# Performance work log

Hardware: AMD Instinct MI355X
Metric: run time of the kernel (lower is better)

## Reference

```python
import jax, jax.numpy as jnp
import numpy as np

N_H = 16
N_KV = 4
D_K = 128
ROPE_BASE = 10000.0


def _rope(t, cos, sin):
    # t: [B, T, H, d_k]; cos/sin: [1, T, 1, d_k//2]
    te, to = t[..., 0::2], t[..., 1::2]
    oe = te * cos - to * sin
    oo = te * sin + to * cos
    return jnp.stack([oe, oo], axis=-1).reshape(t.shape)


def setup_inputs() -> dict:
    key = jax.random.key(0)
    ks = jax.random.split(key, 5)
    B, T, d = 4, 2048, 2048
    s = 0.02
    return {
        "x": jax.random.normal(ks[0], (B, T, d), jnp.float32),
        "Wq": jax.random.normal(ks[1], (d, d), jnp.float32) * s,
        "Wk": jax.random.normal(ks[2], (d, N_KV * D_K), jnp.float32) * s,
        "Wv": jax.random.normal(ks[3], (d, N_KV * D_K), jnp.float32) * s,
        "Wp": jax.random.normal(ks[4], (d, d), jnp.float32) * s,
        "bp": jnp.zeros((d,), jnp.float32),
    }


def reference(x, Wq, Wk, Wv, Wp, bp):
    B, T, C = x.shape
    g = N_H // N_KV  # group size

    q = (x @ Wq).reshape(B, T, N_H, D_K)
    k = (x @ Wk).reshape(B, T, N_KV, D_K)
    v = (x @ Wv).reshape(B, T, N_KV, D_K)

    # RoPE frequencies (constants)
    theta = ROPE_BASE ** (-2.0 * jnp.arange(0, D_K, 2, dtype=jnp.float32) / D_K)
    freq = jnp.arange(T, dtype=jnp.float32)[:, None] * theta[None, :]  # [T, d_k//2]
    cos = jnp.cos(freq)[None, :, None, :]
    sin = jnp.sin(freq)[None, :, None, :]
    q = _rope(q, cos, sin)
    k = _rope(k, cos, sin)

    # GQA: group q heads by shared kv head (equiv to repeat_interleave on kv)
    q = q.reshape(B, T, N_KV, g, D_K).transpose(0, 2, 3, 1, 4)  # [B,n_kv,g,T,d_k]
    k = k.transpose(0, 2, 1, 3)  # [B,n_kv,T,d_k]
    v = v.transpose(0, 2, 1, 3)

    scores = jnp.einsum('bngqd,bnkd->bngqk', q, k) * (D_K ** -0.5)
    causal = jnp.tril(jnp.ones((T, T), bool))
    scores = jnp.where(causal, scores, -jnp.inf)
    attn = jax.nn.softmax(scores, axis=-1)
    out = jnp.einsum('bngqk,bnkd->bngqd', attn, v)  # [B,n_kv,g,T,d_k]
    out = out.transpose(0, 3, 1, 2, 4).reshape(B, T, C)
    return out @ Wp + bp
```

## Files before the change

### kernel.cpp

```cpp
#include <hip/hip_runtime.h>
#include <hip/hip_bf16.h>
#include <math.h>

typedef __bf16 bf16_t;
typedef __bf16 bf16x8 __attribute__((ext_vector_type(8)));
typedef __bf16 bf16x4 __attribute__((ext_vector_type(4)));
typedef float f32x4 __attribute__((ext_vector_type(4)));
typedef float f32x16 __attribute__((ext_vector_type(16)));
typedef unsigned int u32;

#define MFMA16 __builtin_amdgcn_mfma_f32_16x16x32_bf16
#define MFMA32 __builtin_amdgcn_mfma_f32_32x32x16_bf16

static __device__ __forceinline__ u32 pkbf(float a, float b) {
  union { bf16_t h[2]; u32 u; } z;
  z.h[0] = (bf16_t)a; z.h[1] = (bf16_t)b;
  return z.u;
}

static __device__ __forceinline__ void gload16(const bf16_t* g, bf16_t* l) {
  __builtin_amdgcn_global_load_lds(
      (const __attribute__((address_space(1))) void*)g,
      (__attribute__((address_space(3))) void*)l, 16, 0, 0);
}

__global__ void k_f32_to_bf16(const float* __restrict__ in, bf16_t* __restrict__ out, long n) {
  long i = ((long)blockIdx.x * blockDim.x + threadIdx.x) * 4;
  long stride = (long)gridDim.x * blockDim.x * 4;
  for (; i < n; i += stride) {
    const float4 v = *(const float4*)(in + i);
    bf16x4 o; o[0] = (bf16_t)v.x; o[1] = (bf16_t)v.y; o[2] = (bf16_t)v.z; o[3] = (bf16_t)v.w;
    *(bf16x4*)(out + i) = o;
  }
}

__global__ void k_transpose_bf16(const float* __restrict__ W, bf16_t* __restrict__ WT,
                                 int K, int N) {
  __shared__ float tile[32][33];
  int n0 = blockIdx.x * 32, k0 = blockIdx.y * 32;
  int tx = threadIdx.x & 31, ty = threadIdx.x >> 5;
#pragma unroll
  for (int i = 0; i < 4; i++)
    tile[ty + i * 8][tx] = W[(size_t)(k0 + ty + i * 8) * N + n0 + tx];
  __syncthreads();
#pragma unroll
  for (int i = 0; i < 4; i++) {
    int n = ty + i * 8;
    WT[(size_t)(n0 + n) * K + k0 + tx] = (bf16_t)tile[tx][n];
  }
}

__global__ void k_rope(bf16_t* __restrict__ qkv) {
  int idx = blockIdx.x * blockDim.x + threadIdx.x;
  if (idx >= 8192 * 1280) return;
  int r = idx / 1280, p = idx - r * 1280;
  int t = r & 2047;
  int i = p & 63;
  float theta = exp2f(-(float)i * 0.41524101186092029f);
  float f = (float)t * theta;
  float s, c;
  sincosf(f, &s, &c);
  bf16_t* a = qkv + (size_t)r * 3072 + p * 2;
  float e = (float)a[0], o = (float)a[1];
  a[0] = (bf16_t)(e * c - o * s);
  a[1] = (bf16_t)(e * s + o * c);
}

template <bool F32OUT>
__global__ __launch_bounds__(256, 2) void k_gemm_bt(
    const bf16_t* __restrict__ A, const bf16_t* __restrict__ BT,
    bf16_t* __restrict__ Cb, float* __restrict__ Cf,
    const float* __restrict__ bias, int M, int N, int K, int nwg) {
  __shared__ bf16_t sA[128 * 64];
  __shared__ bf16_t sB[128 * 64];
  int nbn = N >> 7;
  int orig = (int)blockIdx.x;
  int swz = (orig & 7) * (nwg >> 3) + (orig >> 3);
  int bm = swz / nbn, bn = swz % nbn;
  int tid = threadIdx.x;
  int lane = tid & 63, wid = tid >> 6;
  int wm = (wid >> 1) << 6, wn = (wid & 1) << 6;
  int lr = lane & 15, lq = lane >> 4;
  f32x4 acc[4][4] = {};

  int srow = wid * 32 + (lane >> 3);
  int scol = (lane & 7) * 8;
  const bf16_t* Ag = A + (size_t)(bm * 128 + srow) * K + scol;
  const bf16_t* Bg = BT + (size_t)(bn * 128 + srow) * K + scol;
  bf16_t* Al = &sA[(wid * 32) * 64];
  bf16_t* Bl = &sB[(wid * 32) * 64];

  for (int k0 = 0; k0 < K; k0 += 64) {
#pragma unroll
    for (int i = 0; i < 4; i++) {
      gload16(Ag + (size_t)i * 8 * K + k0, Al + i * 8 * 64);
      gload16(Bg + (size_t)i * 8 * K + k0, Bl + i * 8 * 64);
    }
    __syncthreads();
#pragma unroll
    for (int kc = 0; kc < 2; kc++) {
      bf16x8 af[4], bfr[4];
#pragma unroll
      for (int m = 0; m < 4; m++)
        af[m] = *(const bf16x8*)&sA[(wm + m * 16 + lr) * 64 + kc * 32 + lq * 8];
#pragma unroll
      for (int n = 0; n < 4; n++)
        bfr[n] = *(const bf16x8*)&sB[(wn + n * 16 + lr) * 64 + kc * 32 + lq * 8];
#pragma unroll
      for (int m = 0; m < 4; m++)
#pragma unroll
        for (int n = 0; n < 4; n++)
          acc[m][n] = MFMA16(af[m], bfr[n], acc[m][n], 0, 0, 0);
    }
    __syncthreads();
  }
#pragma unroll
  for (int m = 0; m < 4; m++) {
    int row0 = bm * 128 + wm + m * 16 + lq * 4;
#pragma unroll
    for (int n = 0; n < 4; n++) {
      int col = bn * 128 + wn + n * 16 + lr;
#pragma unroll
      for (int r = 0; r < 4; r++) {
        if constexpr (F32OUT)
          Cf[(size_t)(row0 + r) * N + col] = acc[m][n][r] + bias[col];
        else
          Cb[(size_t)(row0 + r) * N + col] = (bf16_t)acc[m][n][r];
      }
    }
  }
}

__global__ __launch_bounds__(256, 2) void k_attn(const bf16_t* __restrict__ qkv,
                                                 bf16_t* __restrict__ out) {
  __shared__ bf16_t sK[64 * 128];
  __shared__ bf16_t sVT[128 * 72];
  int bid = blockIdx.x;
  int g = bid >> 6;
  int qt = (g & 1) ? (g >> 1) : (15 - (g >> 1));
  int bh = bid & 63;
  int h = bh & 15, b = bh >> 4;
  int kvh = h >> 2;
  const size_t RS = 3072;
  const bf16_t* Qb = qkv + (size_t)b * 2048 * RS + h * 128;
  const bf16_t* Kb = qkv + (size_t)b * 2048 * RS + 2048 + kvh * 128;
  const bf16_t* Vb = Kb + 512;
  int q0 = qt * 128;
  int tid = threadIdx.x, lane = tid & 63, wid = tid >> 6;
  int l31 = lane & 31, hi = lane >> 5;
  int qw = q0 + wid * 32;

  bf16x8 qf[8];
  {
    const bf16_t* qrow = Qb + (size_t)(qw + l31) * RS + hi * 8;
#pragma unroll
    for (int dc = 0; dc < 8; dc++)
      qf[dc] = *(const bf16x8*)(qrow + dc * 16);
  }

  f32x16 oT[4] = {};
  float m_r = -INFINITY, l_r = 0.f;
  const float SC = 0.08838834764831845f * 1.4426950408889634f;

  int vc = tid & 127, vro = (tid >> 7) * 8;

  int ntiles = 2 * qt + 2;
  for (int kt = 0; kt < ntiles; kt++) {
    int k0 = kt * 64;
#pragma unroll
    for (int ps = 0; ps < 4; ps++) {
      int idx = tid + ps * 256;
      int row = idx >> 4, seg = idx & 15;
      bf16x8 kv = *(const bf16x8*)(Kb + (size_t)(k0 + row) * RS + seg * 8);
      int off = row * 256 + ((seg * 16) ^ ((row & 7) << 4));
      *(bf16x8*)((char*)sK + off) = kv;
    }
#pragma unroll
    for (int i = 0; i < 4; i++) {
      int kr = vro + i * 16;
      bf16x8 vv;
#pragma unroll
      for (int j = 0; j < 8; j++) vv[j] = Vb[(size_t)(k0 + kr + j) * RS + vc];
      *(bf16x8*)&sVT[vc * 72 + kr] = vv;
    }
    __syncthreads();

    if (k0 <= qw + 31) {
      f32x16 sa0 = {}, sa1 = {};
#pragma unroll
      for (int dc = 0; dc < 8; dc++) {
        int cb = (dc * 32 + hi * 16) ^ ((l31 & 7) << 4);
        bf16x8 kf0 = *(const bf16x8*)((const char*)sK + l31 * 256 + cb);
        bf16x8 kf1 = *(const bf16x8*)((const char*)sK + (32 + l31) * 256 + cb);
        sa0 = MFMA32(kf0, qf[dc], sa0, 0, 0, 0);
        sa1 = MFMA32(kf1, qf[dc], sa1, 0, 0, 0);
      }
      float p[2][16];
      int qg = qw + l31;
      float pm = -INFINITY;
#pragma unroll
      for (int nf = 0; nf < 2; nf++)
#pragma unroll
        for (int r = 0; r < 16; r++) {
          int kg = k0 + nf * 32 + (r & 3) + 8 * (r >> 2) + 4 * hi;
          float v = (kg <= qg) ? (nf ? sa1[r] : sa0[r]) * SC : -INFINITY;
          p[nf][r] = v;
          pm = fmaxf(pm, v);
        }
      pm = fmaxf(pm, __shfl_xor(pm, 32));
      bool skip = __all(pm <= m_r + 8.f);
      float mn = skip ? m_r : fmaxf(m_r, pm);
      float alpha = skip ? 1.f : exp2f(m_r - mn);
      m_r = mn;
      float rs = 0.f;
#pragma unroll
      for (int nf = 0; nf < 2; nf++)
#pragma unroll
        for (int r = 0; r < 16; r++) {
          float e = exp2f(p[nf][r] - m_r);
          p[nf][r] = e;
          rs += e;
        }
      rs += __shfl_xor(rs, 32);
      l_r = l_r * alpha + rs;
      if (!skip) {
#pragma unroll
        for (int c = 0; c < 4; c++)
#pragma unroll
          for (int r = 0; r < 16; r++) oT[c][r] *= alpha;
      }
#pragma unroll
      for (int nf = 0; nf < 2; nf++) {
        u32 Qk[4][2];
#pragma unroll
        for (int gg = 0; gg < 4; gg++) {
          Qk[gg][0] = pkbf(p[nf][4 * gg + 0], p[nf][4 * gg + 1]);
          Qk[gg][1] = pkbf(p[nf][4 * gg + 2], p[nf][4 * gg + 3]);
        }
#pragma unroll
        for (int kc = 0; kc < 2; kc++) {
          u32 x0 = __shfl_xor(Qk[2 * kc + 1 - hi][0], 32);
          u32 x1 = __shfl_xor(Qk[2 * kc + 1 - hi][1], 32);
          u32 o0 = Qk[2 * kc + hi][0], o1 = Qk[2 * kc + hi][1];
          union { u32 w[4]; bf16x8 v; } pf;
          pf.w[0] = hi ? x0 : o0;
          pf.w[1] = hi ? x1 : o1;
          pf.w[2] = hi ? o0 : x0;
          pf.w[3] = hi ? o1 : x1;
          int slot = nf * 2 + kc;
#pragma unroll
          for (int c = 0; c < 4; c++) {
            bf16x8 vf = *(const bf16x8*)&sVT[(c * 32 + l31) * 72 + slot * 16 + hi * 8];
            oT[c] = MFMA32(vf, pf.v, oT[c], 0, 0, 0);
          }
        }
      }
    }
    __syncthreads();
  }
  float inv = 1.f / l_r;
  size_t row = (size_t)b * 2048 + qw + l31;
#pragma unroll
  for (int c = 0; c < 4; c++)
#pragma unroll
    for (int rr = 0; rr < 4; rr++) {
      bf16x4 o4;
#pragma unroll
      for (int j = 0; j < 4; j++) o4[j] = (bf16_t)(oT[c][rr * 4 + j] * inv);
      *(bf16x4*)(out + row * 2048 + h * 128 + c * 32 + rr * 8 + hi * 4) = o4;
    }
}

extern "C" void kernel_launch(void* const* d_in, const int* in_sizes, int n_in,
                              void* d_out, int out_size, void* d_ws, size_t ws_size,
                              hipStream_t stream) {
  const float* x = (const float*)d_in[0];
  const float* Wq = (const float*)d_in[1];
  const float* Wk = (const float*)d_in[2];
  const float* Wv = (const float*)d_in[3];
  const float* Wp = (const float*)d_in[4];
  const float* bp = (const float*)d_in[5];
  float* out = (float*)d_out;

  bf16_t* ws = (bf16_t*)d_ws;
  bf16_t* xb = ws;
  bf16_t* qkv = ws + 16777216;
  bf16_t* WqkvT = ws + 16777216 + 25165824;
  bf16_t* WpT = WqkvT + 6291456;

  k_f32_to_bf16<<<2048, 256, 0, stream>>>(x, xb, 16777216L);
  k_transpose_bf16<<<dim3(64, 64), 256, 0, stream>>>(Wq, WqkvT, 2048, 2048);
  k_transpose_bf16<<<dim3(16, 64), 256, 0, stream>>>(Wk, WqkvT + (size_t)2048 * 2048, 2048, 512);
  k_transpose_bf16<<<dim3(16, 64), 256, 0, stream>>>(Wv, WqkvT + (size_t)2560 * 2048, 2048, 512);
  k_transpose_bf16<<<dim3(64, 64), 256, 0, stream>>>(Wp, WpT, 2048, 2048);

  k_gemm_bt<false><<<64 * 24, 256, 0, stream>>>(xb, WqkvT, qkv, nullptr, nullptr, 8192, 3072, 2048, 64 * 24);
  k_rope<<<40960, 256, 0, stream>>>(qkv);
  k_attn<<<1024, 256, 0, stream>>>(qkv, xb);
  k_gemm_bt<true><<<64 * 16, 256, 0, stream>>>(xb, WpT, nullptr, out, bp, 8192, 2048, 2048, 64 * 16);
}
```

Before: 428.0 us.

## Prefetch next K/V tile into registers and streamline softmax in attention loop

Global loads for the next K/V tile are issued into registers right after the barrier, so their latency overlaps with the current tile's MFMA and softmax work. The softmax now skips causal masking on fully unmasked tiles, folds the scale into a single fma before exp2, and uses tree reductions for max and sum. s_setprio raises wave priority around the MFMA blocks. The cost is more live registers (kreg/vreg), which may lower occupancy.

```diff
diff --git a/kernel.cpp b/kernel.cpp
--- a/kernel.cpp
+++ b/kernel.cpp
@@ -162,31 +162,42 @@
   float m_r = -INFINITY, l_r = 0.f;
   const float SC = 0.08838834764831845f * 1.4426950408889634f;
 
+  int k_row = tid >> 4, k_seg = tid & 15;
   int vc = tid & 127, vro = (tid >> 7) * 8;
 
+  bf16x8 kreg[4], vreg[4];
+  auto issue = [&](int k0) {
+#pragma unroll
+    for (int ps = 0; ps < 4; ps++)
+      kreg[ps] = *(const bf16x8*)(Kb + (size_t)(k0 + k_row + ps * 16) * RS + k_seg * 8);
+#pragma unroll
+    for (int i = 0; i < 4; i++) {
+      int kr = vro + i * 16;
+#pragma unroll
+      for (int j = 0; j < 8; j++)
+        vreg[i][j] = Vb[(size_t)(k0 + kr + j) * RS + vc];
+    }
+  };
+
   int ntiles = 2 * qt + 2;
+  issue(0);
   for (int kt = 0; kt < ntiles; kt++) {
     int k0 = kt * 64;
 #pragma unroll
     for (int ps = 0; ps < 4; ps++) {
-      int idx = tid + ps * 256;
-      int row = idx >> 4, seg = idx & 15;
-      bf16x8 kv = *(const bf16x8*)(Kb + (size_t)(k0 + row) * RS + seg * 8);
-      int off = row * 256 + ((seg * 16) ^ ((row & 7) << 4));
-      *(bf16x8*)((char*)sK + off) = kv;
-    }
-#pragma unroll
-    for (int i = 0; i < 4; i++) {
-      int kr = vro + i * 16;
-      bf16x8 vv;
-#pragma unroll
-      for (int j = 0; j < 8; j++) vv[j] = Vb[(size_t)(k0 + kr + j) * RS + vc];
-      *(bf16x8*)&sVT[vc * 72 + kr] = vv;
-    }
+      int row = k_row + ps * 16;
+      int off = row * 256 + ((k_seg * 16) ^ ((row & 7) << 4));
+      *(bf16x8*)((char*)sK + off) = kreg[ps];
+    }
+#pragma unroll
+    for (int i = 0; i < 4; i++)
+      *(bf16x8*)&sVT[vc * 72 + vro + i * 16] = vreg[i];
     __syncthreads();
+    if (kt + 1 < ntiles) issue(k0 + 64);
 
     if (k0 <= qw + 31) {
       f32x16 sa0 = {}, sa1 = {};
+      __builtin_amdgcn_s_setprio(1);
 #pragma unroll
       for (int dc = 0; dc < 8; dc++) {
         int cb = (dc * 32 + hi * 16) ^ ((l31 & 7) << 4);
@@ -195,33 +206,50 @@
         sa0 = MFMA32(kf0, qf[dc], sa0, 0, 0, 0);
         sa1 = MFMA32(kf1, qf[dc], sa1, 0, 0, 0);
       }
+      __builtin_amdgcn_s_setprio(0);
       float p[2][16];
       int qg = qw + l31;
-      float pm = -INFINITY;
-#pragma unroll
-      for (int nf = 0; nf < 2; nf++)
-#pragma unroll
-        for (int r = 0; r < 16; r++) {
-          int kg = k0 + nf * 32 + (r & 3) + 8 * (r >> 2) + 4 * hi;
-          float v = (kg <= qg) ? (nf ? sa1[r] : sa0[r]) * SC : -INFINITY;
-          p[nf][r] = v;
-          pm = fmaxf(pm, v);
-        }
+      if (k0 + 63 <= qw) {
+#pragma unroll
+        for (int r = 0; r < 16; r++) { p[0][r] = sa0[r]; p[1][r] = sa1[r]; }
+      } else {
+#pragma unroll
+        for (int nf = 0; nf < 2; nf++)
+#pragma unroll
+          for (int r = 0; r < 16; r++) {
+            int kg = k0 + nf * 32 + (r & 3) + 8 * (r >> 2) + 4 * hi;
+            p[nf][r] = (kg <= qg) ? (nf ? sa1[r] : sa0[r]) : -INFINITY;
+          }
+      }
+      float mx[16];
+#pragma unroll
+      for (int r = 0; r < 16; r++) mx[r] = fmaxf(p[0][r], p[1][r]);
+#pragma unroll
+      for (int s = 8; s >= 1; s >>= 1)
+#pragma unroll
+        for (int r = 0; r < 8; r++)
+          if (r < s) mx[r] = fmaxf(mx[r], mx[r + s]);
+      float pm = mx[0] * SC;
       pm = fmaxf(pm, __shfl_xor(pm, 32));
       bool skip = __all(pm <= m_r + 8.f);
       float mn = skip ? m_r : fmaxf(m_r, pm);
       float alpha = skip ? 1.f : exp2f(m_r - mn);
       m_r = mn;
-      float rs = 0.f;
+      float nm = -m_r;
 #pragma unroll
       for (int nf = 0; nf < 2; nf++)
 #pragma unroll
-        for (int r = 0; r < 16; r++) {
-          float e = exp2f(p[nf][r] - m_r);
-          p[nf][r] = e;
-          rs += e;
-        }
-      rs += __shfl_xor(rs, 32);
+        for (int r = 0; r < 16; r++)
+          p[nf][r] = exp2f(fmaf(p[nf][r], SC, nm));
+      float sm[16];
+#pragma unroll
+      for (int r = 0; r < 16; r++) sm[r] = p[0][r] + p[1][r];
+#pragma unroll
+      for (int s = 8; s >= 1; s >>= 1)
+#pragma unroll
+        for (int r = 0; r < 8; r++)
+          if (r < s) sm[r] += sm[r + s];
+      float rs = sm[0] + __shfl_xor(sm[0], 32);
       l_r = l_r * alpha + rs;
       if (!skip) {
 #pragma unroll
@@ -248,11 +276,13 @@
           pf.w[2] = hi ? o0 : x0;
           pf.w[3] = hi ? o1 : x1;
           int slot = nf * 2 + kc;
+          __builtin_amdgcn_s_setprio(1);
 #pragma unroll
           for (int c = 0; c < 4; c++) {
             bf16x8 vf = *(const bf16x8*)&sVT[(c * 32 + l31) * 72 + slot * 16 + hi * 8];
             oT[c] = MFMA32(vf, pf.v, oT[c], 0, 0, 0);
           }
+          __builtin_amdgcn_s_setprio(0);
         }
       }
     }
```

New measurement: 433.8 us. Within noise of the previous version (+1.4%).
